# Kernel tuning notes

Measured on AMD Instinct MI355X. Metric: run time of the kernel, lower is better.

## Reference

```python
import jax, jax.numpy as jnp
import numpy as np

B, S, D, E, K = 4, 4096, 2048, 64, 2


def setup_inputs() -> dict:
    key = jax.random.key(0)
    k1, k2 = jax.random.split(key)
    hidden_states = jax.random.normal(k1, (B, S, D), dtype=jnp.float32)
    gate_weight = jax.random.normal(k2, (E, D), dtype=jnp.float32) * 0.02
    return {"hidden_states": hidden_states, "gate_weight": gate_weight}


def reference(hidden_states, gate_weight):
    b, s, d = hidden_states.shape
    e = gate_weight.shape[0]
    n = b * s
    x = hidden_states.reshape(n, d)
    logits = x @ gate_weight.T                                  # [N, E]
    # Original reassigns gate_logits = softmax(gate_logits) in fp32.
    probs = jax.nn.softmax(logits.astype(jnp.float32), axis=-1)  # [N, E]

    top_v, top_i = jax.lax.top_k(probs, K)                       # [N, K]
    top_k_gates = top_v  # normalize_gate_prob_before_dropping=False

    oh = jax.nn.one_hot(top_i, e, dtype=probs.dtype)             # [N, K, E]
    gates = jnp.einsum('nke,nk->ne', oh, top_k_gates)            # scatter of top-k gates

    # Auxiliary losses (training path, use_aux_loss=True)
    gates_mean = gates.mean(axis=0)                              # [E]
    selection_mean = oh.sum(axis=(0, 1)) / n                     # [E]
    load_balancing_loss = (gates_mean * selection_mean).sum() * e
    # NOTE: original computes z-loss on the softmaxed probs (gate_logits was overwritten)
    router_z_loss = (jax.nn.logsumexp(probs, axis=-1) ** 2).mean()

    # torch scatter_ with index [B,S,1,1] only ever writes slot k=0.
    dispatch0 = oh.sum(axis=1).reshape(b, s, e)                  # 1.0 at top-k experts
    combine0 = gates.reshape(b, s, e)
    pad = ((0, 0), (0, 0), (0, 0), (0, K - 1))
    dispatch_tensor = jnp.pad(dispatch0[..., None], pad)         # [B,S,E,K]
    combine_tensor = jnp.pad(combine0[..., None], pad)           # [B,S,E,K]

    return dispatch_tensor, combine_tensor, load_balancing_loss, router_z_loss
```

## Files before the change

### kernel.cpp

```cpp
#include <hip/hip_runtime.h>
#include <hip/hip_bf16.h>
#include <cstddef>

namespace {
constexpr int kD = 2048;
constexpr int kE = 64;
constexpr int kN = 16384;
constexpr size_t kDispatchFloats = (size_t)kN * kE * 2;
constexpr size_t kWsplitOff = 1024;
}

typedef short short8_t __attribute__((ext_vector_type(8)));
typedef float f32x4 __attribute__((ext_vector_type(4)));

__device__ __forceinline__ void split3(float f, unsigned short& s1,
                                       unsigned short& s2, unsigned short& s3) {
  __hip_bfloat16 h1 = __float2bfloat16(f);
  float r1 = f - __bfloat162float(h1);
  __hip_bfloat16 h2 = __float2bfloat16(r1);
  float r2 = r1 - __bfloat162float(h2);
  __hip_bfloat16 h3 = __float2bfloat16(r2);
  s1 = __builtin_bit_cast(unsigned short, h1);
  s2 = __builtin_bit_cast(unsigned short, h2);
  s3 = __builtin_bit_cast(unsigned short, h3);
}

__device__ __forceinline__ void split8(f32x4 a, f32x4 b, short8_t& o1,
                                       short8_t& o2, short8_t& o3) {
  unsigned short s1, s2, s3;
#define SP(v, i, j) \
  split3((v)[i], s1, s2, s3); o1[j]=(short)s1; o2[j]=(short)s2; o3[j]=(short)s3;
  SP(a, 0, 0) SP(a, 1, 1) SP(a, 2, 2) SP(a, 3, 3)
  SP(b, 0, 4) SP(b, 1, 5) SP(b, 2, 6) SP(b, 3, 7)
#undef SP
}

__global__ __launch_bounds__(256)
void prep_kernel(const float* __restrict__ W, unsigned short* __restrict__ img,
                 float* __restrict__ ws) {
  const int t = blockIdx.x * 256 + threadIdx.x;
  if (t < 512) ws[t] = 0.0f;
  const int dq  = t >> 12;
  const int c   = (t >> 9) & 7;
  const int row = (t >> 3) & 63;
  const int cs8 = t & 7;
  const int co  = cs8 ^ (row & 7);
  const float* src = W + (size_t)row * kD + dq * 512 + c * 64 + co * 8;
  const float4 v0 = *reinterpret_cast<const float4*>(src);
  const float4 v1 = *reinterpret_cast<const float4*>(src + 4);
  short8_t o1, o2, o3;
  unsigned short s1, s2, s3;
  split3(v0.x, s1, s2, s3); o1[0]=(short)s1; o2[0]=(short)s2; o3[0]=(short)s3;
  split3(v0.y, s1, s2, s3); o1[1]=(short)s1; o2[1]=(short)s2; o3[1]=(short)s3;
  split3(v0.z, s1, s2, s3); o1[2]=(short)s1; o2[2]=(short)s2; o3[2]=(short)s3;
  split3(v0.w, s1, s2, s3); o1[3]=(short)s1; o2[3]=(short)s2; o3[3]=(short)s3;
  split3(v1.x, s1, s2, s3); o1[4]=(short)s1; o2[4]=(short)s2; o3[4]=(short)s3;
  split3(v1.y, s1, s2, s3); o1[5]=(short)s1; o2[5]=(short)s2; o3[5]=(short)s3;
  split3(v1.z, s1, s2, s3); o1[6]=(short)s1; o2[6]=(short)s2; o3[6]=(short)s3;
  split3(v1.w, s1, s2, s3); o1[7]=(short)s1; o2[7]=(short)s2; o3[7]=(short)s3;
  unsigned short* dst = img + (size_t)(dq * 8 + c) * 12288 + row * 64 + cs8 * 8;
  *reinterpret_cast<short8_t*>(dst + 0 * 4096) = o1;
  *reinterpret_cast<short8_t*>(dst + 1 * 4096) = o2;
  *reinterpret_cast<short8_t*>(dst + 2 * 4096) = o3;
}

__global__ __launch_bounds__(512, 4)
void logits_kernel(const float* __restrict__ x,
                   const unsigned short* __restrict__ wimg,
                   float* __restrict__ out) {
  __shared__ __attribute__((aligned(16))) unsigned char smem[40960];
  float* xsf = reinterpret_cast<float*>(smem);
  unsigned short (*wt)[64][64] =
      reinterpret_cast<unsigned short (*)[64][64]>(smem + 16384);

  const int tid  = threadIdx.x;
  const int lane = tid & 63;
  const int wv   = __builtin_amdgcn_readfirstlane(tid >> 6);
  const int wr   = wv >> 2;
  const int wc   = (wv >> 1) & 1;
  const int kh   = wv & 1;
  const int tile = blockIdx.x & 255;
  const int dq   = blockIdx.x >> 8;
  const int lrow = lane & 15;
  const int lk   = lane >> 4;

  const int row = tid >> 3, seg = tid & 7;
  const float4* __restrict__ bx = reinterpret_cast<const float4*>(x) +
      ((size_t)tile * 64 + row) * 512 + dq * 128 + seg * 2;
  const unsigned short* __restrict__ wbase =
      wimg + (size_t)dq * 8 * 12288 + tid * 8;
  unsigned short* wtf = &wt[0][0][0];
  const int sc0 = ((2 * seg) ^ (row & 15)) * 4;
  const int sc1 = ((2 * seg + 1) ^ (row & 15)) * 4;

  f32x4 acc[2][2];
  const f32x4 z4 = {0.0f, 0.0f, 0.0f, 0.0f};
  acc[0][0] = z4; acc[0][1] = z4; acc[1][0] = z4; acc[1][1] = z4;

  float4 vx0 = bx[0], vx1 = bx[1];

  for (int c = 0; c < 8; ++c) {
    const unsigned short* wsrc = wbase + (size_t)c * 12288;
#pragma unroll
    for (int i = 0; i < 3; ++i)
      __builtin_amdgcn_global_load_lds(
          (const __attribute__((address_space(1))) void*)(wsrc + i * 4096),
          (__attribute__((address_space(3))) void*)(wtf + i * 4096 + wv * 512),
          16, 0, 0);
    __builtin_amdgcn_sched_barrier(0);
    const float4 xa = vx0, xb = vx1;
    const int cn = (c + 1) & 7;
    vx0 = bx[cn * 16 + 0];
    vx1 = bx[cn * 16 + 1];
    *reinterpret_cast<float4*>(xsf + row * 64 + sc0) = xa;
    *reinterpret_cast<float4*>(xsf + row * 64 + sc1) = xb;
    asm volatile("s_waitcnt vmcnt(2) lgkmcnt(0)" ::: "memory");
    __builtin_amdgcn_sched_barrier(0);
    __builtin_amdgcn_s_barrier();
    __builtin_amdgcn_sched_barrier(0);
    {
      const int kc = kh * 4 + lk;
      short8_t b1[2], b2[2], b3[2];
#pragma unroll
      for (int nt = 0; nt < 2; ++nt) {
        const int e = wc * 32 + nt * 16 + lrow;
        const int cw = (kc ^ (e & 7)) * 8;
        b1[nt] = *reinterpret_cast<const short8_t*>(&wt[0][e][cw]);
        b2[nt] = *reinterpret_cast<const short8_t*>(&wt[1][e][cw]);
        b3[nt] = *reinterpret_cast<const short8_t*>(&wt[2][e][cw]);
      }
#pragma unroll
      for (int mt = 0; mt < 2; ++mt) {
        const int ra = wr * 32 + mt * 16 + lrow;
        const int ca0 = ((2 * kc) ^ (ra & 15)) * 4;
        const int ca1 = ((2 * kc + 1) ^ (ra & 15)) * 4;
        const f32x4 va = *reinterpret_cast<const f32x4*>(xsf + ra * 64 + ca0);
        const f32x4 vb = *reinterpret_cast<const f32x4*>(xsf + ra * 64 + ca1);
        short8_t a1, a2, a3;
        split8(va, vb, a1, a2, a3);
#pragma unroll
        for (int nt = 0; nt < 2; ++nt) {
          acc[mt][nt] = __builtin_amdgcn_mfma_f32_16x16x32_bf16(a1, b1[nt], acc[mt][nt], 0, 0, 0);
          acc[mt][nt] = __builtin_amdgcn_mfma_f32_16x16x32_bf16(a1, b2[nt], acc[mt][nt], 0, 0, 0);
          acc[mt][nt] = __builtin_amdgcn_mfma_f32_16x16x32_bf16(a2, b1[nt], acc[mt][nt], 0, 0, 0);
          acc[mt][nt] = __builtin_amdgcn_mfma_f32_16x16x32_bf16(a1, b3[nt], acc[mt][nt], 0, 0, 0);
          acc[mt][nt] = __builtin_amdgcn_mfma_f32_16x16x32_bf16(a3, b1[nt], acc[mt][nt], 0, 0, 0);
          acc[mt][nt] = __builtin_amdgcn_mfma_f32_16x16x32_bf16(a2, b2[nt], acc[mt][nt], 0, 0, 0);
        }
      }
    }
    __builtin_amdgcn_sched_barrier(0);
    __builtin_amdgcn_s_barrier();
  }

  float* __restrict__ mbuf = reinterpret_cast<float*>(smem + 16384);
  if (kh == 1) {
#pragma unroll
    for (int mt = 0; mt < 2; ++mt)
#pragma unroll
      for (int nt = 0; nt < 2; ++nt)
#pragma unroll
        for (int r = 0; r < 4; ++r) {
          const int trow = wr * 32 + mt * 16 + lk * 4 + r;
          const int col  = wc * 32 + nt * 16 + lrow;
          mbuf[trow * 65 + col] = acc[mt][nt][r];
        }
  }
  __syncthreads();
  if (kh == 0) {
    float* __restrict__ base = out + ((dq < 2) ? (size_t)0 : kDispatchFloats);
#pragma unroll
    for (int mt = 0; mt < 2; ++mt)
#pragma unroll
      for (int r = 0; r < 4; ++r) {
        const int trow = wr * 32 + mt * 16 + lk * 4 + r;
        const size_t n = (size_t)tile * 64 + trow;
        float* __restrict__ dst =
            base + n * 128 + (dq & 1) * 64 + wc * 32 + lrow;
#pragma unroll
        for (int nt = 0; nt < 2; ++nt) {
          const int col = wc * 32 + nt * 16 + lrow;
          dst[nt * 16] = acc[mt][nt][r] + mbuf[trow * 65 + col];
        }
      }
  }
}

__global__ __launch_bounds__(256)
void gate_kernel(float* __restrict__ out, float* __restrict__ ws) {
  __shared__ float lg[64][65];
  __shared__ int ti0[64], ti1[64];
  __shared__ float tv0[64], tv1[64], tz2[64];
  const int tid  = threadIdx.x;
  const int tile = blockIdx.x;

  float* __restrict__ outd = out + (size_t)tile * 8192;
  float* __restrict__ outc = out + kDispatchFloats + (size_t)tile * 8192;
  const float4* __restrict__ d4 = reinterpret_cast<const float4*>(outd);
  const float4* __restrict__ c4 = reinterpret_cast<const float4*>(outc);

  const int tq = tid >> 4, q = tid & 15;
#pragma unroll
  for (int k = 0; k < 4; ++k) {
    const int t = k * 16 + tq;
    const float4 a = d4[t * 32 + q];
    const float4 b = d4[t * 32 + 16 + q];
    const float4 c = c4[t * 32 + q];
    const float4 d = c4[t * 32 + 16 + q];
    lg[t][q * 4 + 0] = a.x + b.x + c.x + d.x;
    lg[t][q * 4 + 1] = a.y + b.y + c.y + d.y;
    lg[t][q * 4 + 2] = a.z + b.z + c.z + d.z;
    lg[t][q * 4 + 3] = a.w + b.w + c.w + d.w;
  }
  __syncthreads();

  if (tid < 64) {
    float v0 = -INFINITY, v1 = -INFINITY;
    int i0 = 0, i1 = 0;
    for (int e = 0; e < kE; ++e) {
      const float l = lg[tid][e];
      if (l > v0) { v1 = v0; i1 = i0; v0 = l; i0 = e; }
      else if (l > v1) { v1 = l; i1 = e; }
    }
    const float m = v0;
    float s = 0.0f;
    for (int e = 0; e < kE; ++e) s += __expf(lg[tid][e] - m);
    const float rs = 1.0f / s;
    float zexp = 0.0f;
    for (int e = 0; e < kE; ++e) zexp += __expf(__expf(lg[tid][e] - m) * rs);
    const float z = logf(zexp);
    ti0[tid] = i0; ti1[tid] = i1;
    tv0[tid] = rs;
    tv1[tid] = __expf(v1 - m) * rs;
    tz2[tid] = z * z;
  }
  __syncthreads();

  if (tid < kE) {
    float g = 0.0f, cnt = 0.0f;
    for (int t = 0; t < 64; ++t) {
      if (ti0[t] == tid) { g += tv0[t]; cnt += 1.0f; }
      if (ti1[t] == tid) { g += tv1[t]; cnt += 1.0f; }
    }
    atomicAdd(&ws[tid], g);
    atomicAdd(&ws[kE + tid], cnt);
    float z2 = tz2[tid];
    for (int off = 32; off; off >>= 1) z2 += __shfl_down(z2, off);
    if (tid == 0) atomicAdd(&ws[2 * kE], z2);
  }

  {
    const int t = tid >> 2, sub = tid & 3;
    const int i0 = ti0[t], i1 = ti1[t];
    const float v0 = tv0[t], v1 = tv1[t];
    float4* __restrict__ dp = reinterpret_cast<float4*>(outd) + t * 32;
    float4* __restrict__ cp = reinterpret_cast<float4*>(outc) + t * 32;
#pragma unroll
    for (int j = 0; j < 8; ++j) {
      const int qq = sub * 8 + j;
      const int e0 = qq * 2, e1 = qq * 2 + 1;
      const float d0v = (e0 == i0 || e0 == i1) ? 1.0f : 0.0f;
      const float d1v = (e1 == i0 || e1 == i1) ? 1.0f : 0.0f;
      const float c0 = (e0 == i0) ? v0 : ((e0 == i1) ? v1 : 0.0f);
      const float c1 = (e1 == i0) ? v0 : ((e1 == i1) ? v1 : 0.0f);
      dp[qq] = make_float4(d0v, 0.0f, d1v, 0.0f);
      cp[qq] = make_float4(c0, 0.0f, c1, 0.0f);
    }
  }
}

__global__ void finalize_kernel(const float* __restrict__ ws,
                                float* __restrict__ out) {
  const int e = threadIdx.x;
  float prod = ws[e] * ws[kE + e];
  for (int off = 32; off; off >>= 1) prod += __shfl_down(prod, off);
  if (e == 0) {
    const size_t base = kDispatchFloats * 2;
    const float invN = 1.0f / (float)kN;
    out[base]     = prod * ((float)kE * invN * invN);
    out[base + 1] = ws[2 * kE] * invN;
  }
}

extern "C" void kernel_launch(void* const* d_in, const int* in_sizes, int n_in,
                              void* d_out, int out_size, void* d_ws,
                              size_t ws_size, hipStream_t stream) {
  const float* x = (const float*)d_in[0];
  const float* W = (const float*)d_in[1];
  float* out = (float*)d_out;
  float* ws = (float*)d_ws;
  unsigned short* wimg = (unsigned short*)(ws + kWsplitOff);

  prep_kernel<<<64, 256, 0, stream>>>(W, wimg, ws);
  logits_kernel<<<1024, 512, 0, stream>>>(x, wimg, out);
  gate_kernel<<<256, 256, 0, stream>>>(out, ws);
  finalize_kernel<<<1, kE, 0, stream>>>(ws, out);
}
```

Measured before the change: 73.54 us.

## Load MFMA operands directly from global into registers, dropping LDS staging

The logits GEMM no longer stages x and the split-bf16 weight image through LDS with block barriers. Each wave now loads its MFMA A and B fragments straight from global memory into registers, double-buffered one K-chunk ahead. To make the B loads coalesced, the prep kernel rewrites the weight image in a per-wave fragment order. This removes LDS traffic and the per-iteration barriers, but x rows are now read with strided per-lane loads, wave groups re-read shared data, and register pressure rises from the prefetch buffers.

```diff
diff --git a/kernel.cpp b/kernel.cpp
--- a/kernel.cpp
+++ b/kernel.cpp
@@ -40,12 +40,16 @@
                  float* __restrict__ ws) {
   const int t = blockIdx.x * 256 + threadIdx.x;
   if (t < 512) ws[t] = 0.0f;
-  const int dq  = t >> 12;
-  const int c   = (t >> 9) & 7;
-  const int row = (t >> 3) & 63;
-  const int cs8 = t & 7;
-  const int co  = cs8 ^ (row & 7);
-  const float* src = W + (size_t)row * kD + dq * 512 + c * 64 + co * 8;
+  const int lane = t & 63;
+  const int g    = t >> 6;
+  const int nt   = g & 1;
+  const int wc   = (g >> 1) & 1;
+  const int kh   = (g >> 2) & 1;
+  const int c    = (g >> 3) & 7;
+  const int dq   = g >> 6;
+  const int e = wc * 32 + nt * 16 + (lane & 15);
+  const int k = dq * 512 + c * 64 + kh * 32 + (lane >> 4) * 8;
+  const float* src = W + (size_t)e * kD + k;
   const float4 v0 = *reinterpret_cast<const float4*>(src);
   const float4 v1 = *reinterpret_cast<const float4*>(src + 4);
   short8_t o1, o2, o3;
@@ -58,20 +62,18 @@
   split3(v1.y, s1, s2, s3); o1[5]=(short)s1; o2[5]=(short)s2; o3[5]=(short)s3;
   split3(v1.z, s1, s2, s3); o1[6]=(short)s1; o2[6]=(short)s2; o3[6]=(short)s3;
   split3(v1.w, s1, s2, s3); o1[7]=(short)s1; o2[7]=(short)s2; o3[7]=(short)s3;
-  unsigned short* dst = img + (size_t)(dq * 8 + c) * 12288 + row * 64 + cs8 * 8;
-  *reinterpret_cast<short8_t*>(dst + 0 * 4096) = o1;
-  *reinterpret_cast<short8_t*>(dst + 1 * 4096) = o2;
-  *reinterpret_cast<short8_t*>(dst + 2 * 4096) = o3;
+  const size_t seg = (size_t)((dq * 8 + c) * 2 + kh) * 12;
+  unsigned short* base = img + (seg + (wc * 2 + nt) * 3) * 512 + lane * 8;
+  *reinterpret_cast<short8_t*>(base + 0 * 512) = o1;
+  *reinterpret_cast<short8_t*>(base + 1 * 512) = o2;
+  *reinterpret_cast<short8_t*>(base + 2 * 512) = o3;
 }
 
 __global__ __launch_bounds__(512, 4)
 void logits_kernel(const float* __restrict__ x,
                    const unsigned short* __restrict__ wimg,
                    float* __restrict__ out) {
-  __shared__ __attribute__((aligned(16))) unsigned char smem[40960];
-  float* xsf = reinterpret_cast<float*>(smem);
-  unsigned short (*wt)[64][64] =
-      reinterpret_cast<unsigned short (*)[64][64]>(smem + 16384);
+  __shared__ float mbuf[64 * 65];
 
   const int tid  = threadIdx.x;
   const int lane = tid & 63;
@@ -84,76 +86,69 @@
   const int lrow = lane & 15;
   const int lk   = lane >> 4;
 
-  const int row = tid >> 3, seg = tid & 7;
-  const float4* __restrict__ bx = reinterpret_cast<const float4*>(x) +
-      ((size_t)tile * 64 + row) * 512 + dq * 128 + seg * 2;
-  const unsigned short* __restrict__ wbase =
-      wimg + (size_t)dq * 8 * 12288 + tid * 8;
-  unsigned short* wtf = &wt[0][0][0];
-  const int sc0 = ((2 * seg) ^ (row & 15)) * 4;
-  const int sc1 = ((2 * seg + 1) ^ (row & 15)) * 4;
+  const float* __restrict__ xb0 =
+      x + (size_t)(tile * 64 + wr * 32 + lrow) * kD + dq * 512 + kh * 32 + lk * 8;
+  const float* __restrict__ xb1 = xb0 + (size_t)16 * kD;
+  const unsigned short* __restrict__ wseg =
+      wimg + (size_t)((dq * 8) * 2 + kh) * 12 * 512 + (wc * 2) * 3 * 512 + lane * 8;
+  constexpr int kCStride = 2 * 12 * 512;
 
   f32x4 acc[2][2];
   const f32x4 z4 = {0.0f, 0.0f, 0.0f, 0.0f};
   acc[0][0] = z4; acc[0][1] = z4; acc[1][0] = z4; acc[1][1] = z4;
 
-  float4 vx0 = bx[0], vx1 = bx[1];
-
+  f32x4 xc0, xc1, xc2, xc3, xn0, xn1, xn2, xn3;
+  short8_t bc[6], bn[6];
+
+  xc0 = *reinterpret_cast<const f32x4*>(xb0);
+  xc1 = *reinterpret_cast<const f32x4*>(xb0 + 4);
+  xc2 = *reinterpret_cast<const f32x4*>(xb1);
+  xc3 = *reinterpret_cast<const f32x4*>(xb1 + 4);
+#pragma unroll
+  for (int q = 0; q < 6; ++q)
+    bc[q] = *reinterpret_cast<const short8_t*>(wseg + ((q / 3) * 3 + (q % 3)) * 512);
+
+#pragma unroll 2
   for (int c = 0; c < 8; ++c) {
-    const unsigned short* wsrc = wbase + (size_t)c * 12288;
-#pragma unroll
-    for (int i = 0; i < 3; ++i)
-      __builtin_amdgcn_global_load_lds(
-          (const __attribute__((address_space(1))) void*)(wsrc + i * 4096),
-          (__attribute__((address_space(3))) void*)(wtf + i * 4096 + wv * 512),
-          16, 0, 0);
+    const int cn = (c + 1) & 7;
+    {
+      const float* p0 = xb0 + cn * 64;
+      const float* p1 = xb1 + cn * 64;
+      xn0 = *reinterpret_cast<const f32x4*>(p0);
+      xn1 = *reinterpret_cast<const f32x4*>(p0 + 4);
+      xn2 = *reinterpret_cast<const f32x4*>(p1);
+      xn3 = *reinterpret_cast<const f32x4*>(p1 + 4);
+      const unsigned short* ws2 = wseg + (size_t)cn * kCStride;
+#pragma unroll
+      for (int q = 0; q < 6; ++q)
+        bn[q] = *reinterpret_cast<const short8_t*>(ws2 + ((q / 3) * 3 + (q % 3)) * 512);
+    }
     __builtin_amdgcn_sched_barrier(0);
-    const float4 xa = vx0, xb = vx1;
-    const int cn = (c + 1) & 7;
-    vx0 = bx[cn * 16 + 0];
-    vx1 = bx[cn * 16 + 1];
-    *reinterpret_cast<float4*>(xsf + row * 64 + sc0) = xa;
-    *reinterpret_cast<float4*>(xsf + row * 64 + sc1) = xb;
-    asm volatile("s_waitcnt vmcnt(2) lgkmcnt(0)" ::: "memory");
+    asm volatile("s_waitcnt vmcnt(10)" ::: "memory");
     __builtin_amdgcn_sched_barrier(0);
-    __builtin_amdgcn_s_barrier();
-    __builtin_amdgcn_sched_barrier(0);
-    {
-      const int kc = kh * 4 + lk;
-      short8_t b1[2], b2[2], b3[2];
+#pragma unroll
+    for (int mt = 0; mt < 2; ++mt) {
+      short8_t a1, a2, a3;
+      if (mt == 0) split8(xc0, xc1, a1, a2, a3);
+      else         split8(xc2, xc3, a1, a2, a3);
 #pragma unroll
       for (int nt = 0; nt < 2; ++nt) {
-        const int e = wc * 32 + nt * 16 + lrow;
-        const int cw = (kc ^ (e & 7)) * 8;
-        b1[nt] = *reinterpret_cast<const short8_t*>(&wt[0][e][cw]);
-        b2[nt] = *reinterpret_cast<const short8_t*>(&wt[1][e][cw]);
-        b3[nt] = *reinterpret_cast<const short8_t*>(&wt[2][e][cw]);
+        const short8_t b1 = bc[nt * 3 + 0];
+        const short8_t b2 = bc[nt * 3 + 1];
+        const short8_t b3 = bc[nt * 3 + 2];
+        acc[mt][nt] = __builtin_amdgcn_mfma_f32_16x16x32_bf16(a1, b1, acc[mt][nt], 0, 0, 0);
+        acc[mt][nt] = __builtin_amdgcn_mfma_f32_16x16x32_bf16(a1, b2, acc[mt][nt], 0, 0, 0);
+        acc[mt][nt] = __builtin_amdgcn_mfma_f32_16x16x32_bf16(a2, b1, acc[mt][nt], 0, 0, 0);
+        acc[mt][nt] = __builtin_amdgcn_mfma_f32_16x16x32_bf16(a1, b3, acc[mt][nt], 0, 0, 0);
+        acc[mt][nt] = __builtin_amdgcn_mfma_f32_16x16x32_bf16(a3, b1, acc[mt][nt], 0, 0, 0);
+        acc[mt][nt] = __builtin_amdgcn_mfma_f32_16x16x32_bf16(a2, b2, acc[mt][nt], 0, 0, 0);
       }
-#pragma unroll
-      for (int mt = 0; mt < 2; ++mt) {
-        const int ra = wr * 32 + mt * 16 + lrow;
-        const int ca0 = ((2 * kc) ^ (ra & 15)) * 4;
-        const int ca1 = ((2 * kc + 1) ^ (ra & 15)) * 4;
-        const f32x4 va = *reinterpret_cast<const f32x4*>(xsf + ra * 64 + ca0);
-        const f32x4 vb = *reinterpret_cast<const f32x4*>(xsf + ra * 64 + ca1);
-        short8_t a1, a2, a3;
-        split8(va, vb, a1, a2, a3);
-#pragma unroll
-        for (int nt = 0; nt < 2; ++nt) {
-          acc[mt][nt] = __builtin_amdgcn_mfma_f32_16x16x32_bf16(a1, b1[nt], acc[mt][nt], 0, 0, 0);
-          acc[mt][nt] = __builtin_amdgcn_mfma_f32_16x16x32_bf16(a1, b2[nt], acc[mt][nt], 0, 0, 0);
-          acc[mt][nt] = __builtin_amdgcn_mfma_f32_16x16x32_bf16(a2, b1[nt], acc[mt][nt], 0, 0, 0);
-          acc[mt][nt] = __builtin_amdgcn_mfma_f32_16x16x32_bf16(a1, b3[nt], acc[mt][nt], 0, 0, 0);
-          acc[mt][nt] = __builtin_amdgcn_mfma_f32_16x16x32_bf16(a3, b1[nt], acc[mt][nt], 0, 0, 0);
-          acc[mt][nt] = __builtin_amdgcn_mfma_f32_16x16x32_bf16(a2, b2[nt], acc[mt][nt], 0, 0, 0);
-        }
-      }
-    }
-    __builtin_amdgcn_sched_barrier(0);
-    __builtin_amdgcn_s_barrier();
-  }
-
-  float* __restrict__ mbuf = reinterpret_cast<float*>(smem + 16384);
+    }
+    xc0 = xn0; xc1 = xn1; xc2 = xn2; xc3 = xn3;
+#pragma unroll
+    for (int q = 0; q < 6; ++q) bc[q] = bn[q];
+  }
+
   if (kh == 1) {
 #pragma unroll
     for (int mt = 0; mt < 2; ++mt)
```

New measurement: 85.82 us. +16.7%, slower.
